# Optimization experiments

Hardware: AMD Instinct MI355X
Metric: run time of the kernel (lower is better)

## Reference

```python
import jax, jax.numpy as jnp
import numpy as np

RATIO = 0.5
BN_EPS = 1e-5
L2_EPS = 1e-8


def setup_inputs() -> dict:
    key = jax.random.key(0)
    ks = jax.random.split(key, 8)
    B, L, D, E = 64, 577, 512, 1024
    H = E // 2  # MLP hidden = embed_dim // 2 = 512
    base_features = jax.random.normal(ks[0], (B, L, D), dtype=jnp.float32)
    atten = jax.random.uniform(ks[1], (B, L, L), dtype=jnp.float32)
    s_fc = 1.0 / np.sqrt(D)
    s_h = 1.0 / np.sqrt(H)
    return {
        "base_features": base_features,
        "atten": atten,
        "fc_w": jax.random.uniform(ks[2], (E, D), jnp.float32, -s_fc, s_fc),
        "fc_b": jax.random.uniform(ks[3], (E,), jnp.float32, -s_fc, s_fc),
        "mlp_w0": jax.random.uniform(ks[4], (H, D), jnp.float32, -s_fc, s_fc),
        "mlp_b0": jax.random.uniform(ks[5], (H,), jnp.float32, -s_fc, s_fc),
        "bn0_gamma": jnp.ones((H,), jnp.float32),
        "bn0_beta": jnp.zeros((H,), jnp.float32),
        "mlp_w1": jax.random.uniform(ks[6], (E, H), jnp.float32, -s_h, s_h),
        "mlp_b1": jax.random.uniform(ks[7], (E,), jnp.float32, -s_h, s_h),
    }


def _forward(base_features, atten, fc_w, fc_b, mlp_w0, mlp_b0,
             bn0_gamma, bn0_beta, mlp_w1, mlp_b1):
    B, L, D = base_features.shape
    k = int((L - 1) * RATIO)  # static: derived from shape

    # atten[:, :, 0] = -1; rank tokens by CLS-row attention atten[:, 0]
    scores = atten[:, 0].at[:, 0].set(-1.0)           # [B, L]
    idx = jax.lax.top_k(scores, k)[1]                 # [B, k]

    # gather selected tokens: [B, k, D]
    feats = jnp.take_along_axis(base_features, idx[:, :, None], axis=1)

    # l2norm over last dim (norm = sqrt(sum(x^2)) + eps, then divide)
    norm = jnp.sqrt(jnp.sum(feats * feats, axis=-1, keepdims=True)) + L2_EPS
    feats = feats / norm

    # MLP (num_layers=2): Linear -> BN(training-mode batch stats) -> ReLU -> Linear
    x = feats.reshape(B * k, D)
    h = x @ mlp_w0.T + mlp_b0                         # [B*k, H]
    mu = jnp.mean(h, axis=0)
    var = jnp.mean((h - mu) ** 2, axis=0)             # biased var, as torch BN
    h = jax.nn.relu(bn0_gamma * (h - mu) * jax.lax.rsqrt(var + BN_EPS) + bn0_beta)
    x_att = (h @ mlp_w1.T + mlp_b1).reshape(B, k, -1)  # [B, k, E]

    local = jnp.einsum('bkd,ed->bke', feats, fc_w) + fc_b + x_att

    # maxk_pool1d_var with k=1 and full lengths == max over sequence dim
    return jnp.max(local, axis=1).astype(jnp.float32)  # [B, E]


def reference(base_features, atten, fc_w, fc_b, mlp_w0, mlp_b0,
              bn0_gamma, bn0_beta, mlp_w1, mlp_b1):
    return _forward(base_features, atten, fc_w, fc_b, mlp_w0, mlp_b0,
                    bn0_gamma, bn0_beta, mlp_w1, mlp_b1)
```

## Files before the change

kernel.cpp:

```cpp
#include <hip/hip_runtime.h>
#include <math.h>

#define B_   64
#define L_   577
#define D_   512
#define E_   1024
#define H_   512
#define K_   288
#define N_   (B_ * K_)
#define KBIG 1024
#define MTILES (N_ / 128)

typedef __attribute__((ext_vector_type(8))) __bf16 bf16x8;
typedef __attribute__((ext_vector_type(4))) float f32x4;
typedef __attribute__((ext_vector_type(4))) unsigned short ushort4v;
typedef __attribute__((ext_vector_type(8))) unsigned short ushort8v;

#define OFF_WBIG    0
#define OFF_W0B     2097152
#define OFF_BIASBIG 2621440
#define OFF_SCSH    2625536
#define OFF_IDX     2629632
#define OFF_PSUM    2703360
#define OFF_PSQ     2998272
#define OFF_OUTENC  3293184
#define OFF_ABIG    3555328

static __device__ __forceinline__ unsigned short f2bf(float f) {
  unsigned int u = __builtin_bit_cast(unsigned int, f);
  u = (u + 0x7fffu + ((u >> 16) & 1u)) >> 16;
  return (unsigned short)u;
}
static __device__ __forceinline__ float bf2f(unsigned short s) {
  unsigned int u = ((unsigned int)s) << 16;
  return __builtin_bit_cast(float, u);
}

static __device__ __forceinline__ unsigned int encf(float f) {
  unsigned int u = __builtin_bit_cast(unsigned int, f);
  return (u & 0x80000000u) ? ~u : (u | 0x80000000u);
}
static __device__ __forceinline__ float decf(unsigned int e) {
  unsigned int u = (e & 0x80000000u) ? (e ^ 0x80000000u) : ~e;
  return __builtin_bit_cast(float, u);
}

#define GLOAD_LDS16(g, l)                                          \
  __builtin_amdgcn_global_load_lds(                                \
      (const __attribute__((address_space(1))) void*)(g),          \
      (__attribute__((address_space(3))) void*)(l), 16, 0, 0)

__global__ __launch_bounds__(256) void prep_kernel(
    const float* __restrict__ fc_w, const float* __restrict__ fc_b,
    const float* __restrict__ w0,   const float* __restrict__ w1,
    const float* __restrict__ b1,
    unsigned short* __restrict__ wbig, unsigned short* __restrict__ w0b,
    float* __restrict__ biasbig, unsigned int* __restrict__ outenc) {
  int gid = blockIdx.x * 256 + threadIdx.x;
  if (gid < 65536) outenc[gid] = 0u;
  if (gid < 262144) {
    int e  = gid >> 8;
    int c4 = gid & 255;
    float4 v;
    if (c4 < 128) v = ((const float4*)(fc_w + e * D_))[c4];
    else          v = ((const float4*)(w1   + e * H_))[c4 - 128];
    ushort4v o = { f2bf(v.x), f2bf(v.y), f2bf(v.z), f2bf(v.w) };
    ((ushort4v*)wbig)[gid] = o;
    if (gid < E_) biasbig[gid] = fc_b[gid] + b1[gid];
  } else {
    int idx = gid - 262144;
    float4 v = ((const float4*)w0)[idx];
    ushort4v o = { f2bf(v.x), f2bf(v.y), f2bf(v.z), f2bf(v.w) };
    ((ushort4v*)w0b)[idx] = o;
  }
}

__global__ __launch_bounds__(256) void topk_kernel(
    const float* __restrict__ atten, int* __restrict__ idx) {
  __shared__ float s[L_];
  int b = blockIdx.x;
  const float* row = atten + (size_t)b * L_ * L_;
  for (int i = threadIdx.x; i < L_; i += 256) s[i] = (i == 0) ? -1.0f : row[i];
  __syncthreads();
  for (int i = threadIdx.x; i < L_; i += 256) {
    float si = s[i];
    int rank = 0;
    for (int j = 0; j < L_; ++j) {
      float sj = s[j];
      rank += (sj > si) || (sj == si && j < i);
    }
    if (rank < K_) idx[b * K_ + rank] = i;
  }
}

__global__ __launch_bounds__(128) void gather_norm_kernel(
    const float* __restrict__ base, const int* __restrict__ idx,
    unsigned short* __restrict__ abig) {
  int r = blockIdx.x;
  int b = r / K_;
  int tok = idx[r];
  const float* src = base + ((size_t)b * L_ + tok) * D_;
  float4 v = ((const float4*)src)[threadIdx.x];
  float ss = v.x * v.x + v.y * v.y + v.z * v.z + v.w * v.w;
  #pragma unroll
  for (int o = 32; o > 0; o >>= 1) ss += __shfl_down(ss, o, 64);
  __shared__ float wsum[2];
  if ((threadIdx.x & 63) == 0) wsum[threadIdx.x >> 6] = ss;
  __syncthreads();
  float total = wsum[0] + wsum[1];
  float inv = 1.0f / (sqrtf(total) + 1e-8f);
  ushort4v o4 = { f2bf(v.x * inv), f2bf(v.y * inv), f2bf(v.z * inv), f2bf(v.w * inv) };
  ((ushort4v*)(abig + (size_t)r * KBIG))[threadIdx.x] = o4;
}

template <int MODE>
__global__ __launch_bounds__(256) void gemm_mfma_kernel(
    const unsigned short* __restrict__ A, int lda,
    const unsigned short* __restrict__ W, int ldw,
    const float* __restrict__ bias,
    unsigned short* __restrict__ Cbf, int ldc, int K,
    float* __restrict__ psum, float* __restrict__ psq,
    unsigned int* __restrict__ outenc) {
  __shared__ unsigned short As[128 * 64];
  __shared__ unsigned short Bs[128 * 64];
  __shared__ float s_sum[4][64];
  __shared__ float s_sq[4][64];
  const int tid  = threadIdx.x;
  const int wave = tid >> 6;
  const int lane = tid & 63;
  const int m0 = blockIdx.x * 128;
  const int n0 = blockIdx.y * 128;

  const int srow = wave * 8 + (lane >> 3);
  const int g8   = ((lane & 7) ^ ((lane >> 3) & 7)) * 8;
  const int ldst = (wave * 64 + lane) * 8;

  const int quad = lane >> 4;
  const int l15  = lane & 15;
  const int wm = (wave & 1) * 64;
  const int wn = (wave >> 1) * 64;
  const int slot0 = quad ^ (l15 & 7);

  f32x4 acc[4][4];
  #pragma unroll
  for (int i = 0; i < 4; ++i)
    #pragma unroll
    for (int j = 0; j < 4; ++j)
      acc[i][j] = (f32x4)(0.0f);

  for (int k0 = 0; k0 < K; k0 += 64) {
    #pragma unroll
    for (int q = 0; q < 4; ++q) {
      GLOAD_LDS16(A + (size_t)(m0 + q * 32 + srow) * lda + k0 + g8,
                  &As[q * 2048 + ldst]);
      GLOAD_LDS16(W + (size_t)(n0 + q * 32 + srow) * ldw + k0 + g8,
                  &Bs[q * 2048 + ldst]);
    }
    __syncthreads();
    #pragma unroll
    for (int kk = 0; kk < 2; ++kk) {
      const int slot = slot0 ^ (kk * 4);
      bf16x8 af[4], bfr[4];
      #pragma unroll
      for (int i = 0; i < 4; ++i)
        af[i] = *(const bf16x8*)&As[(wm + 16 * i + l15) * 64 + slot * 8];
      #pragma unroll
      for (int j = 0; j < 4; ++j)
        bfr[j] = *(const bf16x8*)&Bs[(wn + 16 * j + l15) * 64 + slot * 8];
      #pragma unroll
      for (int i = 0; i < 4; ++i)
        #pragma unroll
        for (int j = 0; j < 4; ++j)
          acc[i][j] = __builtin_amdgcn_mfma_f32_16x16x32_bf16(af[i], bfr[j], acc[i][j], 0, 0, 0);
    }
    __syncthreads();
  }

  if (MODE == 0) {
    #pragma unroll
    for (int j = 0; j < 4; ++j) {
      int col = n0 + wn + 16 * j + l15;
      float bb = bias[col];
      float sm = 0.f, sq = 0.f;
      #pragma unroll
      for (int i = 0; i < 4; ++i) {
        int row_base = m0 + wm + 16 * i + quad * 4;
        #pragma unroll
        for (int r = 0; r < 4; ++r) {
          float v = acc[i][j][r] + bb;
          Cbf[(size_t)(row_base + r) * ldc + col] = f2bf(v);
          sm += v; sq += v * v;
        }
      }
      sm += __shfl_xor(sm, 16, 64); sm += __shfl_xor(sm, 32, 64);
      sq += __shfl_xor(sq, 16, 64); sq += __shfl_xor(sq, 32, 64);
      if (quad == 0) { s_sum[wave][j * 16 + l15] = sm; s_sq[wave][j * 16 + l15] = sq; }
    }
    __syncthreads();
    if (tid < 128) {
      int half = tid >> 6;
      int c = tid & 63;
      float sm = s_sum[half * 2][c] + s_sum[half * 2 + 1][c];
      float sq = s_sq[half * 2][c] + s_sq[half * 2 + 1][c];
      int col = n0 + half * 64 + c;
      psum[blockIdx.x * H_ + col] = sm;
      psq [blockIdx.x * H_ + col] = sq;
    }
  } else {
    #pragma unroll
    for (int j = 0; j < 4; ++j) {
      int col = n0 + wn + 16 * j + l15;
      float bb = bias[col];
      float m[4];
      #pragma unroll
      for (int i = 0; i < 4; ++i) {
        float v = fmaxf(fmaxf(acc[i][j][0], acc[i][j][1]),
                        fmaxf(acc[i][j][2], acc[i][j][3]));
        m[i] = v + bb;
      }
      #pragma unroll
      for (int i = 0; i < 4; ++i) {
        m[i] = fmaxf(m[i], __shfl_xor(m[i], 16, 64));
        m[i] = fmaxf(m[i], __shfl_xor(m[i], 32, 64));
      }
      if (quad == 0) {
        int base = m0 + wm;
        int b0i = (base) / K_;
        float cur = m[0]; int cb = b0i;
        #pragma unroll
        for (int i = 1; i < 4; ++i) {
          int bi = (base + 16 * i) / K_;
          if (bi == cb) cur = fmaxf(cur, m[i]);
          else { atomicMax(&outenc[cb * E_ + col], encf(cur)); cur = m[i]; cb = bi; }
        }
        atomicMax(&outenc[cb * E_ + col], encf(cur));
      }
    }
  }
}

__global__ __launch_bounds__(256) void bn_stats2_kernel(
    const float* __restrict__ psum, const float* __restrict__ psq,
    const float* __restrict__ gamma, const float* __restrict__ beta,
    float* __restrict__ scsh) {
  __shared__ float ls[8][32], lq[8][32];
  int c32 = threadIdx.x & 31;
  int slice = threadIdx.x >> 5;
  int c = blockIdx.x * 32 + c32;
  float S = 0.f, Q = 0.f;
  for (int i = 0; i < 18; ++i) {
    int mx = slice * 18 + i;
    S += psum[mx * H_ + c];
    Q += psq [mx * H_ + c];
  }
  ls[slice][c32] = S; lq[slice][c32] = Q;
  __syncthreads();
  if (slice == 0) {
    float St = 0.f, Qt = 0.f;
    #pragma unroll
    for (int s = 0; s < 8; ++s) { St += ls[s][c32]; Qt += lq[s][c32]; }
    const float invN = 1.0f / (float)N_;
    float mu = St * invN;
    float var = Qt * invN - mu * mu;
    float sc = rsqrtf(var + 1e-5f) * gamma[c];
    scsh[c] = sc;
    scsh[512 + c] = beta[c] - mu * sc;
  }
}

__global__ __launch_bounds__(256) void bn_apply_kernel(
    unsigned short* __restrict__ abig, const float* __restrict__ scsh) {
  int gid = blockIdx.x * 256 + threadIdx.x;
  int r = gid >> 6;
  int c8 = gid & 63;
  int c = c8 * 8;
  ushort8v* p = (ushort8v*)(abig + (size_t)r * KBIG + H_) + c8;
  ushort8v v = *p;
  float4 sca = *(const float4*)&scsh[c];
  float4 scb = *(const float4*)&scsh[c + 4];
  float4 sha = *(const float4*)&scsh[512 + c];
  float4 shb = *(const float4*)&scsh[512 + c + 4];
  float sc[8] = {sca.x, sca.y, sca.z, sca.w, scb.x, scb.y, scb.z, scb.w};
  float sh[8] = {sha.x, sha.y, sha.z, sha.w, shb.x, shb.y, shb.z, shb.w};
  ushort8v o;
  #pragma unroll
  for (int j = 0; j < 8; ++j) {
    float x = bf2f(v[j]);
    o[j] = f2bf(fmaxf(x * sc[j] + sh[j], 0.0f));
  }
  *p = o;
}

__global__ __launch_bounds__(256) void decode_kernel(
    const unsigned int* __restrict__ outenc, float* __restrict__ out) {
  int gid = blockIdx.x * 256 + threadIdx.x;
  out[gid] = decf(outenc[gid]);
}

extern "C" void kernel_launch(void* const* d_in, const int* in_sizes, int n_in,
                              void* d_out, int out_size, void* d_ws, size_t ws_size,
                              hipStream_t stream) {
  const float* base  = (const float*)d_in[0];
  const float* atten = (const float*)d_in[1];
  const float* fc_w  = (const float*)d_in[2];
  const float* fc_b  = (const float*)d_in[3];
  const float* w0    = (const float*)d_in[4];
  const float* b0    = (const float*)d_in[5];
  const float* gamma = (const float*)d_in[6];
  const float* beta  = (const float*)d_in[7];
  const float* w1    = (const float*)d_in[8];
  const float* b1    = (const float*)d_in[9];
  float* out = (float*)d_out;

  char* ws = (char*)d_ws;
  unsigned short* wbig    = (unsigned short*)(ws + OFF_WBIG);
  unsigned short* w0b     = (unsigned short*)(ws + OFF_W0B);
  float*          biasbig = (float*)(ws + OFF_BIASBIG);
  float*          scsh    = (float*)(ws + OFF_SCSH);
  int*            idx     = (int*)  (ws + OFF_IDX);
  float*          psum    = (float*)(ws + OFF_PSUM);
  float*          psq     = (float*)(ws + OFF_PSQ);
  unsigned int*   outenc  = (unsigned int*)(ws + OFF_OUTENC);
  unsigned short* abig    = (unsigned short*)(ws + OFF_ABIG);

  prep_kernel<<<1280, 256, 0, stream>>>(fc_w, fc_b, w0, w1, b1, wbig, w0b,
                                        biasbig, outenc);
  topk_kernel<<<B_, 256, 0, stream>>>(atten, idx);
  gather_norm_kernel<<<N_, 128, 0, stream>>>(base, idx, abig);
  {
    dim3 grid(MTILES, H_ / 128);
    gemm_mfma_kernel<0><<<grid, 256, 0, stream>>>(abig, KBIG, w0b, D_, b0,
                                                  abig + H_, KBIG, D_,
                                                  psum, psq, nullptr);
  }
  bn_stats2_kernel<<<16, 256, 0, stream>>>(psum, psq, gamma, beta, scsh);
  bn_apply_kernel<<<(N_ * 64) / 256, 256, 0, stream>>>(abig, scsh);
  {
    dim3 grid(MTILES, E_ / 128);
    gemm_mfma_kernel<1><<<grid, 256, 0, stream>>>(abig, KBIG, wbig, KBIG, biasbig,
                                                  nullptr, 0, KBIG, nullptr, nullptr,
                                                  outenc);
  }
  decode_kernel<<<(B_ * E_) / 256, 256, 0, stream>>>(outenc, out);
}
```

Baseline: 292.8 us.

## Fuse whole pipeline into one cooperative persistent kernel with grid syncs

```diff
diff --git a/kernel.cpp b/kernel.cpp
--- a/kernel.cpp
+++ b/kernel.cpp
@@ -1,5 +1,8 @@
 #include <hip/hip_runtime.h>
+#include <hip/hip_cooperative_groups.h>
 #include <math.h>
+
+namespace cg = cooperative_groups;
 
 #define B_   64
 #define L_   577
@@ -10,6 +13,8 @@
 #define N_   (B_ * K_)
 #define KBIG 1024
 #define MTILES (N_ / 128)
+#define GRID_ 576
+#define NTHREADS (GRID_ * 256)
 
 typedef __attribute__((ext_vector_type(8))) __bf16 bf16x8;
 typedef __attribute__((ext_vector_type(4))) float f32x4;
@@ -22,9 +27,9 @@
 #define OFF_SCSH    2625536
 #define OFF_IDX     2629632
 #define OFF_PSUM    2703360
-#define OFF_PSQ     2998272
-#define OFF_OUTENC  3293184
-#define OFF_ABIG    3555328
+#define OFF_PSQ     2705408
+#define OFF_OUTENC  2707456
+#define OFF_ABIG    2969600
 
 static __device__ __forceinline__ unsigned short f2bf(float f) {
   unsigned int u = __builtin_bit_cast(unsigned int, f);
@@ -35,7 +40,6 @@
   unsigned int u = ((unsigned int)s) << 16;
   return __builtin_bit_cast(float, u);
 }
-
 static __device__ __forceinline__ unsigned int encf(float f) {
   unsigned int u = __builtin_bit_cast(unsigned int, f);
   return (u & 0x80000000u) ? ~u : (u | 0x80000000u);
@@ -49,15 +53,290 @@
   __builtin_amdgcn_global_load_lds(                                \
       (const __attribute__((address_space(1))) void*)(g),          \
       (__attribute__((address_space(3))) void*)(l), 16, 0, 0)
+
+template <int MODE>
+static __device__ __forceinline__ void gemm_tile(
+    const unsigned short* __restrict__ A, int lda,
+    const unsigned short* __restrict__ W, int ldw,
+    const float* __restrict__ bias,
+    unsigned short* __restrict__ Cbf, int ldc, int K,
+    float* __restrict__ psum, float* __restrict__ psq,
+    unsigned int* __restrict__ outenc,
+    char* smem, int m0, int n0) {
+  unsigned short* As = (unsigned short*)smem;
+  unsigned short* Bs = As + 8192;
+  const int tid  = threadIdx.x;
+  const int wave = tid >> 6;
+  const int lane = tid & 63;
+
+  const int srow = wave * 8 + (lane >> 3);
+  const int g8   = ((lane & 7) ^ ((lane >> 3) & 7)) * 8;
+  const int ldst = (wave * 64 + lane) * 8;
+
+  const int quad = lane >> 4;
+  const int l15  = lane & 15;
+  const int wm = (wave & 1) * 64;
+  const int wn = (wave >> 1) * 64;
+  const int slot0 = quad ^ (l15 & 7);
+
+  f32x4 acc[4][4];
+  #pragma unroll
+  for (int i = 0; i < 4; ++i)
+    #pragma unroll
+    for (int j = 0; j < 4; ++j)
+      acc[i][j] = (f32x4)(0.0f);
+
+  for (int k0 = 0; k0 < K; k0 += 64) {
+    #pragma unroll
+    for (int q = 0; q < 4; ++q) {
+      GLOAD_LDS16(A + (size_t)(m0 + q * 32 + srow) * lda + k0 + g8,
+                  &As[q * 2048 + ldst]);
+      GLOAD_LDS16(W + (size_t)(n0 + q * 32 + srow) * ldw + k0 + g8,
+                  &Bs[q * 2048 + ldst]);
+    }
+    __syncthreads();
+    #pragma unroll
+    for (int kk = 0; kk < 2; ++kk) {
+      const int slot = slot0 ^ (kk * 4);
+      bf16x8 af[4], bfr[4];
+      #pragma unroll
+      for (int i = 0; i < 4; ++i)
+        af[i] = *(const bf16x8*)&As[(wm + 16 * i + l15) * 64 + slot * 8];
+      #pragma unroll
+      for (int j = 0; j < 4; ++j)
+        bfr[j] = *(const bf16x8*)&Bs[(wn + 16 * j + l15) * 64 + slot * 8];
+      #pragma unroll
+      for (int i = 0; i < 4; ++i)
+        #pragma unroll
+        for (int j = 0; j < 4; ++j)
+          acc[i][j] = __builtin_amdgcn_mfma_f32_16x16x32_bf16(af[i], bfr[j], acc[i][j], 0, 0, 0);
+    }
+    __syncthreads();
+  }
+
+  if (MODE == 0) {
+    float* s_sum = (float*)smem;
+    float* s_sq  = s_sum + 256;
+    #pragma unroll
+    for (int j = 0; j < 4; ++j) {
+      int col = n0 + wn + 16 * j + l15;
+      float bb = bias[col];
+      float sm = 0.f, sq = 0.f;
+      #pragma unroll
+      for (int i = 0; i < 4; ++i) {
+        int row_base = m0 + wm + 16 * i + quad * 4;
+        #pragma unroll
+        for (int r = 0; r < 4; ++r) {
+          float v = acc[i][j][r] + bb;
+          Cbf[(size_t)(row_base + r) * ldc + col] = f2bf(v);
+          sm += v; sq += v * v;
+        }
+      }
+      sm += __shfl_xor(sm, 16, 64); sm += __shfl_xor(sm, 32, 64);
+      sq += __shfl_xor(sq, 16, 64); sq += __shfl_xor(sq, 32, 64);
+      if (quad == 0) { s_sum[wave * 64 + j * 16 + l15] = sm;
+                       s_sq [wave * 64 + j * 16 + l15] = sq; }
+    }
+    __syncthreads();
+    if (tid < 128) {
+      int half = tid >> 6;
+      int c = tid & 63;
+      float sm = s_sum[half * 128 + c] + s_sum[half * 128 + 64 + c];
+      float sq = s_sq [half * 128 + c] + s_sq [half * 128 + 64 + c];
+      int col = n0 + half * 64 + c;
+      atomicAdd(&psum[col], sm);
+      atomicAdd(&psq [col], sq);
+    }
+    __syncthreads();
+  } else {
+    #pragma unroll
+    for (int j = 0; j < 4; ++j) {
+      int col = n0 + wn + 16 * j + l15;
+      float bb = bias[col];
+      float m[4];
+      #pragma unroll
+      for (int i = 0; i < 4; ++i) {
+        float v = fmaxf(fmaxf(acc[i][j][0], acc[i][j][1]),
+                        fmaxf(acc[i][j][2], acc[i][j][3]));
+        m[i] = v + bb;
+      }
+      #pragma unroll
+      for (int i = 0; i < 4; ++i) {
+        m[i] = fmaxf(m[i], __shfl_xor(m[i], 16, 64));
+        m[i] = fmaxf(m[i], __shfl_xor(m[i], 32, 64));
+      }
+      if (quad == 0) {
+        int base = m0 + wm;
+        float cur = m[0]; int cb = base / K_;
+        #pragma unroll
+        for (int i = 1; i < 4; ++i) {
+          int bi = (base + 16 * i) / K_;
+          if (bi == cb) cur = fmaxf(cur, m[i]);
+          else { atomicMax(&outenc[cb * E_ + col], encf(cur)); cur = m[i]; cb = bi; }
+        }
+        atomicMax(&outenc[cb * E_ + col], encf(cur));
+      }
+    }
+  }
+}
+
+static __device__ __forceinline__ void topk_block(
+    const float* __restrict__ atten, int* __restrict__ idx, int b,
+    float* s, int tid) {
+  const float* row = atten + (size_t)b * L_ * L_;
+  for (int i = tid; i < L_; i += 256) s[i] = (i == 0) ? -1.0f : row[i];
+  __syncthreads();
+  for (int i = tid; i < L_; i += 256) {
+    float si = s[i];
+    int rank = 0;
+    for (int j = 0; j < L_; ++j) {
+      float sj = s[j];
+      rank += (sj > si) || (sj == si && j < i);
+    }
+    if (rank < K_) idx[b * K_ + rank] = i;
+  }
+  __syncthreads();
+}
+
+static __device__ __forceinline__ void bn_coef(
+    const float* psum, const float* psq, const float* gamma,
+    const float* beta, float* scsh, int c) {
+  const float invN = 1.0f / (float)N_;
+  float mu = psum[c] * invN;
+  float var = psq[c] * invN - mu * mu;
+  float sc = rsqrtf(var + 1e-5f) * gamma[c];
+  scsh[c] = sc;
+  scsh[512 + c] = beta[c] - mu * sc;
+}
+
+__global__ __launch_bounds__(256, 3) void mega_kernel(
+    const float* __restrict__ base, const float* __restrict__ atten,
+    const float* __restrict__ fc_w, const float* __restrict__ fc_b,
+    const float* __restrict__ w0,   const float* __restrict__ b0,
+    const float* __restrict__ gamma, const float* __restrict__ beta,
+    const float* __restrict__ w1,   const float* __restrict__ b1,
+    float* __restrict__ out, char* __restrict__ ws) {
+  __shared__ __align__(16) char smem[32768];
+  cg::grid_group grid = cg::this_grid();
+
+  unsigned short* wbig    = (unsigned short*)(ws + OFF_WBIG);
+  unsigned short* w0b     = (unsigned short*)(ws + OFF_W0B);
+  float*          biasbig = (float*)(ws + OFF_BIASBIG);
+  float*          scsh    = (float*)(ws + OFF_SCSH);
+  int*            idx     = (int*)  (ws + OFF_IDX);
+  float*          psum    = (float*)(ws + OFF_PSUM);
+  float*          psq     = (float*)(ws + OFF_PSQ);
+  unsigned int*   outenc  = (unsigned int*)(ws + OFF_OUTENC);
+  unsigned short* abig    = (unsigned short*)(ws + OFF_ABIG);
+
+  const int blk = blockIdx.x;
+  const int tid = threadIdx.x;
+
+  for (int gid = blk * 256 + tid; gid < 327680; gid += NTHREADS) {
+    if (gid < 65536) outenc[gid] = 0u;
+    if (gid < 512) { psum[gid] = 0.f; psq[gid] = 0.f; }
+    if (gid < E_) biasbig[gid] = fc_b[gid] + b1[gid];
+    if (gid < 262144) {
+      int e  = gid >> 8;
+      int c4 = gid & 255;
+      float4 v;
+      if (c4 < 128) v = ((const float4*)(fc_w + e * D_))[c4];
+      else          v = ((const float4*)(w1   + e * H_))[c4 - 128];
+      ushort4v o = { f2bf(v.x), f2bf(v.y), f2bf(v.z), f2bf(v.w) };
+      ((ushort4v*)wbig)[gid] = o;
+    } else {
+      int i2 = gid - 262144;
+      float4 v = ((const float4*)w0)[i2];
+      ushort4v o = { f2bf(v.x), f2bf(v.y), f2bf(v.z), f2bf(v.w) };
+      ((ushort4v*)w0b)[i2] = o;
+    }
+  }
+  if (blk >= GRID_ - B_) topk_block(atten, idx, blk - (GRID_ - B_), (float*)smem, tid);
+  __threadfence();
+  grid.sync();
+
+  {
+    float* gw = (float*)smem;
+    const int half = tid >> 7;
+    const int t128 = tid & 127;
+    const int wv   = tid >> 6;
+    for (int it = 0; it < 16; ++it) {
+      int r = blk * 32 + it * 2 + half;
+      int b = r / K_;
+      int tok = idx[r];
+      const float* src = base + ((size_t)b * L_ + tok) * D_;
+      float4 v = ((const float4*)src)[t128];
+      float ss = v.x * v.x + v.y * v.y + v.z * v.z + v.w * v.w;
+      #pragma unroll
+      for (int o = 32; o > 0; o >>= 1) ss += __shfl_down(ss, o, 64);
+      if ((tid & 63) == 0) gw[wv] = ss;
+      __syncthreads();
+      float total = gw[2 * half] + gw[2 * half + 1];
+      float inv = 1.0f / (sqrtf(total) + 1e-8f);
+      ushort4v o4 = { f2bf(v.x * inv), f2bf(v.y * inv),
+                      f2bf(v.z * inv), f2bf(v.w * inv) };
+      ((ushort4v*)(abig + (size_t)r * KBIG))[t128] = o4;
+      __syncthreads();
+    }
+  }
+  __threadfence();
+  grid.sync();
+
+  {
+    int m0 = (blk % MTILES) * 128;
+    int n0 = (blk / MTILES) * 128;
+    gemm_tile<0>(abig, KBIG, w0b, D_, b0, abig + H_, KBIG, D_,
+                 psum, psq, nullptr, smem, m0, n0);
+  }
+  __threadfence();
+  grid.sync();
+
+  if (blk == 0)
+    for (int c = tid; c < H_; c += 256) bn_coef(psum, psq, gamma, beta, scsh, c);
+  __threadfence();
+  grid.sync();
+
+  for (int gid = blk * 256 + tid; gid < N_ * 64; gid += NTHREADS) {
+    int r = gid >> 6;
+    int c8 = gid & 63;
+    int c = c8 * 8;
+    ushort8v* p = (ushort8v*)(abig + (size_t)r * KBIG + H_) + c8;
+    ushort8v v = *p;
+    ushort8v o;
+    #pragma unroll
+    for (int j = 0; j < 8; ++j) {
+      float x = bf2f(v[j]);
+      o[j] = f2bf(fmaxf(x * scsh[c + j] + scsh[512 + c + j], 0.0f));
+    }
+    *p = o;
+  }
+  __threadfence();
+  grid.sync();
+
+  for (int t = blk; t < MTILES * 8; t += GRID_) {
+    int m0 = (t % MTILES) * 128;
+    int n0 = (t / MTILES) * 128;
+    gemm_tile<1>(abig, KBIG, wbig, KBIG, biasbig, nullptr, 0, KBIG,
+                 nullptr, nullptr, outenc, smem, m0, n0);
+  }
+  __threadfence();
+  grid.sync();
+
+  for (int gid = blk * 256 + tid; gid < B_ * E_; gid += NTHREADS)
+    out[gid] = decf(outenc[gid]);
+}
 
 __global__ __launch_bounds__(256) void prep_kernel(
     const float* __restrict__ fc_w, const float* __restrict__ fc_b,
     const float* __restrict__ w0,   const float* __restrict__ w1,
     const float* __restrict__ b1,
     unsigned short* __restrict__ wbig, unsigned short* __restrict__ w0b,
-    float* __restrict__ biasbig, unsigned int* __restrict__ outenc) {
+    float* __restrict__ biasbig, unsigned int* __restrict__ outenc,
+    float* __restrict__ psum, float* __restrict__ psq) {
   int gid = blockIdx.x * 256 + threadIdx.x;
   if (gid < 65536) outenc[gid] = 0u;
+  if (gid < 512) { psum[gid] = 0.f; psq[gid] = 0.f; }
+  if (gid < E_) biasbig[gid] = fc_b[gid] + b1[gid];
   if (gid < 262144) {
     int e  = gid >> 8;
     int c4 = gid & 255;
@@ -66,31 +345,18 @@
     else          v = ((const float4*)(w1   + e * H_))[c4 - 128];
     ushort4v o = { f2bf(v.x), f2bf(v.y), f2bf(v.z), f2bf(v.w) };
     ((ushort4v*)wbig)[gid] = o;
-    if (gid < E_) biasbig[gid] = fc_b[gid] + b1[gid];
   } else {
-    int idx = gid - 262144;
-    float4 v = ((const float4*)w0)[idx];
+    int i2 = gid - 262144;
+    float4 v = ((const float4*)w0)[i2];
     ushort4v o = { f2bf(v.x), f2bf(v.y), f2bf(v.z), f2bf(v.w) };
-    ((ushort4v*)w0b)[idx] = o;
+    ((ushort4v*)w0b)[i2] = o;
   }
 }
 
 __global__ __launch_bounds__(256) void topk_kernel(
     const float* __restrict__ atten, int* __restrict__ idx) {
   __shared__ float s[L_];
-  int b = blockIdx.x;
-  const float* row = atten + (size_t)b * L_ * L_;
-  for (int i = threadIdx.x; i < L_; i += 256) s[i] = (i == 0) ? -1.0f : row[i];
-  __syncthreads();
-  for (int i = threadIdx.x; i < L_; i += 256) {
-    float si = s[i];
-    int rank = 0;
-    for (int j = 0; j < L_; ++j) {
-      float sj = s[j];
-      rank += (sj > si) || (sj == si && j < i);
-    }
-    if (rank < K_) idx[b * K_ + rank] = i;
-  }
+  topk_block(atten, idx, blockIdx.x, s, threadIdx.x);
 }
 
 __global__ __launch_bounds__(128) void gather_norm_kernel(
@@ -113,159 +379,21 @@
   ((ushort4v*)(abig + (size_t)r * KBIG))[threadIdx.x] = o4;
 }
 
-template <int MODE>
-__global__ __launch_bounds__(256) void gemm_mfma_kernel(
-    const unsigned short* __restrict__ A, int lda,
-    const unsigned short* __restrict__ W, int ldw,
-    const float* __restrict__ bias,
-    unsigned short* __restrict__ Cbf, int ldc, int K,
-    float* __restrict__ psum, float* __restrict__ psq,
-    unsigned int* __restrict__ outenc) {
-  __shared__ unsigned short As[128 * 64];
-  __shared__ unsigned short Bs[128 * 64];
-  __shared__ float s_sum[4][64];
-  __shared__ float s_sq[4][64];
-  const int tid  = threadIdx.x;
-  const int wave = tid >> 6;
-  const int lane = tid & 63;
-  const int m0 = blockIdx.x * 128;
-  const int n0 = blockIdx.y * 128;
-
-  const int srow = wave * 8 + (lane >> 3);
-  const int g8   = ((lane & 7) ^ ((lane >> 3) & 7)) * 8;
-  const int ldst = (wave * 64 + lane) * 8;
-
-  const int quad = lane >> 4;
-  const int l15  = lane & 15;
-  const int wm = (wave & 1) * 64;
-  const int wn = (wave >> 1) * 64;
-  const int slot0 = quad ^ (l15 & 7);
-
-  f32x4 acc[4][4];
-  #pragma unroll
-  for (int i = 0; i < 4; ++i)
-    #pragma unroll
-    for (int j = 0; j < 4; ++j)
-      acc[i][j] = (f32x4)(0.0f);
-
-  for (int k0 = 0; k0 < K; k0 += 64) {
-    #pragma unroll
-    for (int q = 0; q < 4; ++q) {
-      GLOAD_LDS16(A + (size_t)(m0 + q * 32 + srow) * lda + k0 + g8,
-                  &As[q * 2048 + ldst]);
-      GLOAD_LDS16(W + (size_t)(n0 + q * 32 + srow) * ldw + k0 + g8,
-                  &Bs[q * 2048 + ldst]);
-    }
-    __syncthreads();
-    #pragma unroll
-    for (int kk = 0; kk < 2; ++kk) {
-      const int slot = slot0 ^ (kk * 4);
-      bf16x8 af[4], bfr[4];
-      #pragma unroll
-      for (int i = 0; i < 4; ++i)
-        af[i] = *(const bf16x8*)&As[(wm + 16 * i + l15) * 64 + slot * 8];
-      #pragma unroll
-      for (int j = 0; j < 4; ++j)
-        bfr[j] = *(const bf16x8*)&Bs[(wn + 16 * j + l15) * 64 + slot * 8];
-      #pragma unroll
-      for (int i = 0; i < 4; ++i)
-        #pragma unroll
-        for (int j = 0; j < 4; ++j)
-          acc[i][j] = __builtin_amdgcn_mfma_f32_16x16x32_bf16(af[i], bfr[j], acc[i][j], 0, 0, 0);
-    }
-    __syncthreads();
-  }
-
-  if (MODE == 0) {
-    #pragma unroll
-    for (int j = 0; j < 4; ++j) {
-      int col = n0 + wn + 16 * j + l15;
-      float bb = bias[col];
-      float sm = 0.f, sq = 0.f;
-      #pragma unroll
-      for (int i = 0; i < 4; ++i) {
-        int row_base = m0 + wm + 16 * i + quad * 4;
-        #pragma unroll
-        for (int r = 0; r < 4; ++r) {
-          float v = acc[i][j][r] + bb;
-          Cbf[(size_t)(row_base + r) * ldc + col] = f2bf(v);
-          sm += v; sq += v * v;
-        }
-      }
-      sm += __shfl_xor(sm, 16, 64); sm += __shfl_xor(sm, 32, 64);
-      sq += __shfl_xor(sq, 16, 64); sq += __shfl_xor(sq, 32, 64);
-      if (quad == 0) { s_sum[wave][j * 16 + l15] = sm; s_sq[wave][j * 16 + l15] = sq; }
-    }
-    __syncthreads();
-    if (tid < 128) {
-      int half = tid >> 6;
-      int c = tid & 63;
-      float sm = s_sum[half * 2][c] + s_sum[half * 2 + 1][c];
-      float sq = s_sq[half * 2][c] + s_sq[half * 2 + 1][c];
-      int col = n0 + half * 64 + c;
-      psum[blockIdx.x * H_ + col] = sm;
-      psq [blockIdx.x * H_ + col] = sq;
-    }
-  } else {
-    #pragma unroll
-    for (int j = 0; j < 4; ++j) {
-      int col = n0 + wn + 16 * j + l15;
-      float bb = bias[col];
-      float m[4];
-      #pragma unroll
-      for (int i = 0; i < 4; ++i) {
-        float v = fmaxf(fmaxf(acc[i][j][0], acc[i][j][1]),
-                        fmaxf(acc[i][j][2], acc[i][j][3]));
-        m[i] = v + bb;
-      }
-      #pragma unroll
-      for (int i = 0; i < 4; ++i) {
-        m[i] = fmaxf(m[i], __shfl_xor(m[i], 16, 64));
-        m[i] = fmaxf(m[i], __shfl_xor(m[i], 32, 64));
-      }
-      if (quad == 0) {
-        int base = m0 + wm;
-        int b0i = (base) / K_;
-        float cur = m[0]; int cb = b0i;
-        #pragma unroll
-        for (int i = 1; i < 4; ++i) {
-          int bi = (base + 16 * i) / K_;
-          if (bi == cb) cur = fmaxf(cur, m[i]);
-          else { atomicMax(&outenc[cb * E_ + col], encf(cur)); cur = m[i]; cb = bi; }
-        }
-        atomicMax(&outenc[cb * E_ + col], encf(cur));
-      }
-    }
-  }
+__global__ __launch_bounds__(256) void gemm0_kernel(
+    unsigned short* __restrict__ abig, const unsigned short* __restrict__ w0b,
+    const float* __restrict__ b0, float* __restrict__ psum,
+    float* __restrict__ psq) {
+  __shared__ __align__(16) char smem[32768];
+  gemm_tile<0>(abig, KBIG, w0b, D_, b0, abig + H_, KBIG, D_,
+               psum, psq, nullptr, smem, blockIdx.x * 128, blockIdx.y * 128);
 }
 
 __global__ __launch_bounds__(256) void bn_stats2_kernel(
     const float* __restrict__ psum, const float* __restrict__ psq,
     const float* __restrict__ gamma, const float* __restrict__ beta,
     float* __restrict__ scsh) {
-  __shared__ float ls[8][32], lq[8][32];
-  int c32 = threadIdx.x & 31;
-  int slice = threadIdx.x >> 5;
-  int c = blockIdx.x * 32 + c32;
-  float S = 0.f, Q = 0.f;
-  for (int i = 0; i < 18; ++i) {
-    int mx = slice * 18 + i;
-    S += psum[mx * H_ + c];
-    Q += psq [mx * H_ + c];
-  }
-  ls[slice][c32] = S; lq[slice][c32] = Q;
-  __syncthreads();
-  if (slice == 0) {
-    float St = 0.f, Qt = 0.f;
-    #pragma unroll
-    for (int s = 0; s < 8; ++s) { St += ls[s][c32]; Qt += lq[s][c32]; }
-    const float invN = 1.0f / (float)N_;
-    float mu = St * invN;
-    float var = Qt * invN - mu * mu;
-    float sc = rsqrtf(var + 1e-5f) * gamma[c];
-    scsh[c] = sc;
-    scsh[512 + c] = beta[c] - mu * sc;
-  }
+  int c = blockIdx.x * 256 + threadIdx.x;
+  bn_coef(psum, psq, gamma, beta, scsh, c);
 }
 
 __global__ __launch_bounds__(256) void bn_apply_kernel(
@@ -276,19 +404,20 @@
   int c = c8 * 8;
   ushort8v* p = (ushort8v*)(abig + (size_t)r * KBIG + H_) + c8;
   ushort8v v = *p;
-  float4 sca = *(const float4*)&scsh[c];
-  float4 scb = *(const float4*)&scsh[c + 4];
-  float4 sha = *(const float4*)&scsh[512 + c];
-  float4 shb = *(const float4*)&scsh[512 + c + 4];
-  float sc[8] = {sca.x, sca.y, sca.z, sca.w, scb.x, scb.y, scb.z, scb.w};
-  float sh[8] = {sha.x, sha.y, sha.z, sha.w, shb.x, shb.y, shb.z, shb.w};
   ushort8v o;
   #pragma unroll
-  for (int j = 0; j < 8; ++j) {
-    float x = bf2f(v[j]);
-    o[j] = f2bf(fmaxf(x * sc[j] + sh[j], 0.0f));
-  }
+  for (int j = 0; j < 8; ++j)
+    o[j] = f2bf(fmaxf(bf2f(v[j]) * scsh[c + j] + scsh[512 + c + j], 0.0f));
   *p = o;
+}
+
+__global__ __launch_bounds__(256) void gemm1_kernel(
+    const unsigned short* __restrict__ abig,
+    const unsigned short* __restrict__ wbig,
+    const float* __restrict__ biasbig, unsigned int* __restrict__ outenc) {
+  __shared__ __align__(16) char smem[32768];
+  gemm_tile<1>(abig, KBIG, wbig, KBIG, biasbig, nullptr, 0, KBIG,
+               nullptr, nullptr, outenc, smem, blockIdx.x * 128, blockIdx.y * 128);
 }
 
 __global__ __launch_bounds__(256) void decode_kernel(
@@ -311,35 +440,38 @@
   const float* w1    = (const float*)d_in[8];
   const float* b1    = (const float*)d_in[9];
   float* out = (float*)d_out;
-
   char* ws = (char*)d_ws;
-  unsigned short* wbig    = (unsigned short*)(ws + OFF_WBIG);
-  unsigned short* w0b     = (unsigned short*)(ws + OFF_W0B);
-  float*          biasbig = (float*)(ws + OFF_BIASBIG);
-  float*          scsh    = (float*)(ws + OFF_SCSH);
-  int*            idx     = (int*)  (ws + OFF_IDX);
-  float*          psum    = (float*)(ws + OFF_PSUM);
-  float*          psq     = (float*)(ws + OFF_PSQ);
-  unsigned int*   outenc  = (unsigned int*)(ws + OFF_OUTENC);
-  unsigned short* abig    = (unsigned short*)(ws + OFF_ABIG);
-
-  prep_kernel<<<1280, 256, 0, stream>>>(fc_w, fc_b, w0, w1, b1, wbig, w0b,
-                                        biasbig, outenc);
-  topk_kernel<<<B_, 256, 0, stream>>>(atten, idx);
-  gather_norm_kernel<<<N_, 128, 0, stream>>>(base, idx, abig);
-  {
-    dim3 grid(MTILES, H_ / 128);
-    gemm_mfma_kernel<0><<<grid, 256, 0, stream>>>(abig, KBIG, w0b, D_, b0,
-                                                  abig + H_, KBIG, D_,
-                                                  psum, psq, nullptr);
-  }
-  bn_stats2_kernel<<<16, 256, 0, stream>>>(psum, psq, gamma, beta, scsh);
-  bn_apply_kernel<<<(N_ * 64) / 256, 256, 0, stream>>>(abig, scsh);
-  {
-    dim3 grid(MTILES, E_ / 128);
-    gemm_mfma_kernel<1><<<grid, 256, 0, stream>>>(abig, KBIG, wbig, KBIG, biasbig,
-                                                  nullptr, 0, KBIG, nullptr, nullptr,
-                                                  outenc);
-  }
-  decode_kernel<<<(B_ * E_) / 256, 256, 0, stream>>>(outenc, out);
-}
+
+  void* args[] = {
+    (void*)&base, (void*)&atten, (void*)&fc_w, (void*)&fc_b,
+    (void*)&w0, (void*)&b0, (void*)&gamma, (void*)&beta,
+    (void*)&w1, (void*)&b1, (void*)&out, (void*)&ws,
+  };
+  hipError_t err = hipLaunchCooperativeKernel((const void*)mega_kernel,
+                                              dim3(GRID_), dim3(256), args, 0,
+                                              stream);
+  if (err != hipSuccess) {
+    (void)hipGetLastError();
+    unsigned short* wbig    = (unsigned short*)(ws + OFF_WBIG);
+    unsigned short* w0b     = (unsigned short*)(ws + OFF_W0B);
+    float*          biasbig = (float*)(ws + OFF_BIASBIG);
+    float*          scsh    = (float*)(ws + OFF_SCSH);
+    int*            idx     = (int*)  (ws + OFF_IDX);
+    float*          psum    = (float*)(ws + OFF_PSUM);
+    float*          psq     = (float*)(ws + OFF_PSQ);
+    unsigned int*   outenc  = (unsigned int*)(ws + OFF_OUTENC);
+    unsigned short* abig    = (unsigned short*)(ws + OFF_ABIG);
+
+    prep_kernel<<<1280, 256, 0, stream>>>(fc_w, fc_b, w0, w1, b1, wbig, w0b,
+                                          biasbig, outenc, psum, psq);
+    topk_kernel<<<B_, 256, 0, stream>>>(atten, idx);
+    gather_norm_kernel<<<N_, 128, 0, stream>>>(base, idx, abig);
+    gemm0_kernel<<<dim3(MTILES, H_ / 128), 256, 0, stream>>>(abig, w0b, b0,
+                                                             psum, psq);
+    bn_stats2_kernel<<<2, 256, 0, stream>>>(psum, psq, gamma, beta, scsh);
+    bn_apply_kernel<<<(N_ * 64) / 256, 256, 0, stream>>>(abig, scsh);
+    gemm1_kernel<<<dim3(MTILES, E_ / 128), 256, 0, stream>>>(abig, wbig,
+                                                             biasbig, outenc);
+    decode_kernel<<<(B_ * E_) / 256, 256, 0, stream>>>(outenc, out);
+  }
+}
```

Result: slower. 991.6 us (+238.7%).
